# Kernel tuning notes

Hardware: AMD Instinct MI355X
Metric: run time of the kernel (lower is better)

Reference implementation:

```python
import jax, jax.numpy as jnp
import numpy as np

B, S, D, H = 2, 2048, 2048, 32
HD = D // H  # head_dim = 64
NEG = -1e10


def setup_inputs() -> dict:
    key = jax.random.key(0)
    k1, k2, k3 = jax.random.split(key, 3)
    hidden_states = jax.random.normal(k1, (B, S, D), dtype=jnp.float32)
    W = jax.random.normal(k2, (D, 3 * D), dtype=jnp.float32) * (1.0 / np.sqrt(D))
    b = jax.random.normal(k3, (3 * D,), dtype=jnp.float32) * 0.02
    return {"hidden_states": hidden_states, "W": W, "b": b}


def reference(hidden_states, W, b):
    # fused QKV projection: [B,S,D] @ [D,3D] -> [B,S,3D]
    qvk = hidden_states @ W + b
    # OPT interleaved layout: reshape to [B,S,D,3]; channel 0=q, 1=v, 2=k
    qvk = qvk.reshape(B, S, D, 3)
    q = qvk[..., 0].reshape(B, S, H, HD)
    v = qvk[..., 1].reshape(B, S, H, HD)
    k = qvk[..., 2].reshape(B, S, H, HD)
    # causal bias: -1e10 strictly above diagonal, shape [1,1,S,S]
    bias = jnp.triu(jnp.full((S, S), NEG, dtype=jnp.float32), 1)[None, None]
    # dot_product_attention_weights: scale q by 1/sqrt(head_dim)
    scale = jnp.asarray(1.0 / np.sqrt(HD), dtype=jnp.float32)
    scores = jnp.einsum('bqhd,bkhd->bhqk', q * scale, k) + bias  # [B,H,S,S]
    attn_weights = jax.nn.softmax(scores, axis=-1)
    attn_output = jnp.einsum('bhqk,bkhd->bqhd', attn_weights, v)  # [B,S,H,HD]
    return attn_output.reshape(B, S, D)
```

## Files before the change

### kernel.cpp

```cpp
#include <hip/hip_runtime.h>
#include <hip/hip_bf16.h>
#include <stdint.h>

typedef unsigned short ushort_t;
typedef __bf16 bf16x8 __attribute__((ext_vector_type(8)));
typedef float f32x4 __attribute__((ext_vector_type(4)));
typedef float f32x16 __attribute__((ext_vector_type(16)));
typedef int int4v __attribute__((ext_vector_type(4)));
typedef ushort_t ushort8 __attribute__((ext_vector_type(8)));

__device__ __forceinline__ ushort_t f2bf(float f) {
  union { float f; unsigned int u; } v; v.f = f;
  unsigned int r = v.u + 0x7fffu + ((v.u >> 16) & 1u);
  return (ushort_t)(r >> 16);
}

__device__ __forceinline__ bf16x8 ld_bf8(const ushort_t* p) {
  return *reinterpret_cast<const bf16x8*>(p);
}

__device__ __forceinline__ void g2lds16(const void* g, void* l) {
  __builtin_amdgcn_global_load_lds(
      (const __attribute__((address_space(1))) unsigned int*)g,
      (__attribute__((address_space(3))) unsigned int*)l,
      16, 0, 0);
}

__device__ __forceinline__ float ex2(float x) { return __builtin_amdgcn_exp2f(x); }

__device__ __forceinline__ int cvtpk(float a, float b) {
  int r;
  asm("v_cvt_pk_bf16_f32 %0, %1, %2" : "=v"(r) : "v"(a), "v"(b));
  return r;
}

__global__ __launch_bounds__(256) void cvt_hs(const float* __restrict__ in,
                                              ushort_t* __restrict__ out) {
  int i = (blockIdx.x * 256 + threadIdx.x) * 8;
  float4 a = *reinterpret_cast<const float4*>(in + i);
  float4 b = *reinterpret_cast<const float4*>(in + i + 4);
  ushort8 r;
  r[0] = f2bf(a.x); r[1] = f2bf(a.y); r[2] = f2bf(a.z); r[3] = f2bf(a.w);
  r[4] = f2bf(b.x); r[5] = f2bf(b.y); r[6] = f2bf(b.z); r[7] = f2bf(b.w);
  *reinterpret_cast<ushort8*>(out + i) = r;
}

__global__ __launch_bounds__(256) void transpose_W(const float* __restrict__ Win,
                                                   ushort_t* __restrict__ Wt) {
  __shared__ ushort_t T[64][65];
  const int t = threadIdx.x;
  const int k0 = (blockIdx.x & 31) * 64;
  const int n0 = (blockIdx.x >> 5) * 64;
#pragma unroll
  for (int i = 0; i < 16; ++i) {
    int idx = i * 256 + t;
    int r = idx >> 6, c = idx & 63;
    T[r][c] = f2bf(Win[(k0 + r) * 6144 + n0 + c]);
  }
  __syncthreads();
#pragma unroll
  for (int i = 0; i < 16; ++i) {
    int idx = i * 256 + t;
    int nr = idx >> 6, kc = idx & 63;
    Wt[(n0 + nr) * 2048 + k0 + kc] = T[kc][nr];
  }
}

__global__ __launch_bounds__(256, 2) void gemm_qkv(
    const ushort_t* __restrict__ A, const ushort_t* __restrict__ Bt,
    const float* __restrict__ bias,
    ushort_t* __restrict__ Qb, ushort_t* __restrict__ Kb,
    ushort_t* __restrict__ VT) {
  __shared__ __align__(16) char smem[25600];
  ushort_t* As = (ushort_t*)smem;
  ushort_t* Bs = (ushort_t*)(smem + 8192);
  ushort_t* Cs = (ushort_t*)smem;
  const int t = threadIdx.x;
  const int w = t >> 6, l = t & 63;
  const int lo = l & 15, hi = l >> 4;
  const int wr = w >> 1, wc = w & 1;

  int bid = blockIdx.x;
  int swz = (bid & 7) * 128 + (bid >> 3);
  const int mt = swz & 31, nt = swz >> 5;
  const int bm = mt * 128;
  const int bn = nt * 192;

  f32x4 acc[4][6];
#pragma unroll
  for (int i = 0; i < 4; ++i)
#pragma unroll
    for (int j = 0; j < 6; ++j) acc[i][j] = f32x4{0.f, 0.f, 0.f, 0.f};

  const ushort_t* Ag = A + (size_t)bm * 2048;
  const ushort_t* Bg = Bt + (size_t)bn * 2048;

  for (int kk = 0; kk < 2048; kk += 32) {
#pragma unroll
    for (int r2 = 0; r2 < 2; ++r2) {
      int c = r2 * 256 + t;
      int row = c >> 2, s4 = c & 3;
      int slot = s4 ^ ((row & 3) ^ ((row >> 2) & 3));
      g2lds16(Ag + row * 2048 + kk + slot * 8, As + c * 8);
    }
#pragma unroll
    for (int r3 = 0; r3 < 3; ++r3) {
      int c = r3 * 256 + t;
      int row = c >> 2, s4 = c & 3;
      int slot = s4 ^ ((row & 3) ^ ((row >> 2) & 3));
      g2lds16(Bg + row * 2048 + kk + slot * 8, Bs + c * 8);
    }
    __syncthreads();
    bf16x8 af[4], bfr[6];
#pragma unroll
    for (int mf = 0; mf < 4; ++mf) {
      int row = wr * 64 + mf * 16 + lo;
      int fr = (row & 3) ^ ((row >> 2) & 3);
      af[mf] = ld_bf8(As + row * 32 + ((hi ^ fr) << 3));
    }
#pragma unroll
    for (int nf = 0; nf < 6; ++nf) {
      int row = wc * 96 + nf * 16 + lo;
      int fr = (row & 3) ^ ((row >> 2) & 3);
      bfr[nf] = ld_bf8(Bs + row * 32 + ((hi ^ fr) << 3));
    }
    __builtin_amdgcn_s_setprio(1);
#pragma unroll
    for (int mf = 0; mf < 4; ++mf)
#pragma unroll
      for (int nf = 0; nf < 6; ++nf)
        acc[mf][nf] = __builtin_amdgcn_mfma_f32_16x16x32_bf16(
            af[mf], bfr[nf], acc[mf][nf], 0, 0, 0);
    __builtin_amdgcn_s_setprio(0);
    __syncthreads();
  }

  float bv[6];
  int ch[6];
#pragma unroll
  for (int nf = 0; nf < 6; ++nf) {
    int nl = wc * 96 + nf * 16 + lo;
    bv[nf] = bias[bn + nl];
    ch[nf] = nl % 3;
  }
  const int b_ = bm >> 11;
  const int bh = (b_ << 5) + nt;
  const float QS = 0.125f * 1.44269504f;

#pragma unroll
  for (int h = 0; h < 2; ++h) {
    if (wr == h) {
#pragma unroll
      for (int mf = 0; mf < 4; ++mf)
#pragma unroll
        for (int nf = 0; nf < 6; ++nf) {
          int rloc = mf * 16 + hi * 4;
          int nl = wc * 96 + nf * 16 + lo;
          f32x4 a = acc[mf][nf];
#pragma unroll
          for (int j = 0; j < 4; ++j) {
            float v = a[j] + bv[nf];
            if (ch[nf] == 0) v *= QS;
            Cs[(rloc + j) * 200 + nl] = f2bf(v);
          }
        }
    }
    __syncthreads();
    const int sbase = (bm & 2047) + h * 64;
#pragma unroll
    for (int it = 0; it < 2; ++it) {
      int slot = it * 256 + t;
      int r = slot >> 3, g = slot & 7;
      ushort8 vq, vk;
#pragma unroll
      for (int u = 0; u < 8; ++u) {
        int hd = g * 8 + u;
        vq[u] = Cs[r * 200 + hd * 3];
        vk[u] = Cs[r * 200 + hd * 3 + 2];
      }
      size_t rowoff = ((size_t)bh * 2048 + sbase + r) * 64 + g * 8;
      *reinterpret_cast<ushort8*>(Qb + rowoff) = vq;
      *reinterpret_cast<ushort8*>(Kb + rowoff) = vk;
    }
#pragma unroll
    for (int it = 0; it < 2; ++it) {
      int slot = it * 256 + t;
      int hd = slot >> 3, sg = slot & 7;
      ushort8 vv;
#pragma unroll
      for (int u = 0; u < 8; ++u) vv[u] = Cs[(sg * 8 + u) * 200 + hd * 3 + 1];
      *reinterpret_cast<ushort8*>(VT + ((size_t)bh * 64 + hd) * 2048 + sbase +
                                  sg * 8) = vv;
    }
    __syncthreads();
  }
}

__global__ __launch_bounds__(64) void attn(
    const ushort_t* __restrict__ Qb, const ushort_t* __restrict__ Kb,
    const ushort_t* __restrict__ VT, float* __restrict__ out) {
  __shared__ float Ld[32 * 66];
  const int l = threadIdx.x;
  const int ql = l & 31, hi = l >> 5;

  const int bid = blockIdx.x;
  const int bh = bid & 63;
  const int qt = 63 - (bid >> 6);
  const int q0 = qt * 32;
  const int nch = qt + 1;

  const ushort_t* qp = Qb + (bh * 2048 + q0 + ql) * 64 + hi * 8;
  bf16x8 qf[4];
#pragma unroll
  for (int dc = 0; dc < 4; ++dc) qf[dc] = ld_bf8(qp + dc * 16);

  f32x16 o0, o1;
#pragma unroll
  for (int r = 0; r < 16; ++r) { o0[r] = 0.f; o1[r] = 0.f; }
  float mr = -1e30f, lr = 0.f;

  const ushort_t* kbase = Kb + bh * 2048 * 64 + hi * 8;
  const ushort_t* vbase = VT + (bh * 64 + ql) * 2048 + hi * 8;

  bf16x8 kf[4], vf0[2], vf1[2];
  {
    const ushort_t* kp = kbase + ql * 64;
#pragma unroll
    for (int dc = 0; dc < 4; ++dc) kf[dc] = ld_bf8(kp + dc * 16);
#pragma unroll
    for (int s = 0; s < 2; ++s) {
      const ushort_t* vp = vbase + s * 16;
      vf0[s] = ld_bf8(vp);
      vf1[s] = ld_bf8(vp + 32 * 2048);
    }
  }

  for (int c = 0; c < nch; ++c) {
    const int cn = (c + 1 < nch) ? (c + 1) : c;
    const ushort_t* kpn = kbase + (cn * 32 + ql) * 64;
    bf16x8 kn[4], vn0[2], vn1[2];
#pragma unroll
    for (int dc = 0; dc < 4; ++dc) kn[dc] = ld_bf8(kpn + dc * 16);
#pragma unroll
    for (int s = 0; s < 2; ++s) {
      const ushort_t* vpn = vbase + cn * 32 + s * 16;
      vn0[s] = ld_bf8(vpn);
      vn1[s] = ld_bf8(vpn + 32 * 2048);
    }

    f32x16 p;
#pragma unroll
    for (int r = 0; r < 16; ++r) p[r] = 0.f;
    __builtin_amdgcn_s_setprio(1);
#pragma unroll
    for (int dc = 0; dc < 4; ++dc)
      p = __builtin_amdgcn_mfma_f32_32x32x16_bf16(kf[dc], qf[dc], p, 0, 0, 0);
    __builtin_amdgcn_s_setprio(0);
    if (c == nch - 1) {
#pragma unroll
      for (int r = 0; r < 16; ++r) {
        int kvr = (r & 3) + 8 * (r >> 2) + 4 * hi;
        if (kvr > ql) p[r] = -1e30f;
      }
    }
    float mx = p[0];
#pragma unroll
    for (int r = 1; r < 16; ++r) mx = fmaxf(mx, p[r]);
    mx = fmaxf(mx, __shfl_xor(mx, 32));
    if (__any(mx > mr + 10.0f)) {
      float mn = fmaxf(mr, mx);
      float scl = ex2(mr - mn);
      mr = mn;
      lr *= scl;
#pragma unroll
      for (int r = 0; r < 16; ++r) { o0[r] *= scl; o1[r] *= scl; }
    }
    float sum = 0.f;
#pragma unroll
    for (int r = 0; r < 16; ++r) {
      p[r] = ex2(p[r] - mr);
      sum += p[r];
    }
    sum += __shfl_xor(sum, 32);
    lr += sum;

    __builtin_amdgcn_s_setprio(1);
#pragma unroll
    for (int s = 0; s < 2; ++s) {
      int x0 = cvtpk(p[8 * s + 0], p[8 * s + 1]);
      int x1 = cvtpk(p[8 * s + 2], p[8 * s + 3]);
      int y0 = cvtpk(p[8 * s + 4], p[8 * s + 5]);
      int y1 = cvtpk(p[8 * s + 6], p[8 * s + 7]);
      int ox0 = __shfl_xor(x0, 32);
      int ox1 = __shfl_xor(x1, 32);
      int oy0 = __shfl_xor(y0, 32);
      int oy1 = __shfl_xor(y1, 32);
      int4v wv;
      wv[0] = hi ? oy0 : x0;
      wv[1] = hi ? oy1 : x1;
      wv[2] = hi ? y0 : ox0;
      wv[3] = hi ? y1 : ox1;
      bf16x8 pf = __builtin_bit_cast(bf16x8, wv);
      o0 = __builtin_amdgcn_mfma_f32_32x32x16_bf16(vf0[s], pf, o0, 0, 0, 0);
      o1 = __builtin_amdgcn_mfma_f32_32x32x16_bf16(vf1[s], pf, o1, 0, 0, 0);
    }
    __builtin_amdgcn_s_setprio(0);
#pragma unroll
    for (int dc = 0; dc < 4; ++dc) kf[dc] = kn[dc];
#pragma unroll
    for (int s = 0; s < 2; ++s) {
      vf0[s] = vn0[s];
      vf1[s] = vn1[s];
    }
  }

  const float inv = 1.0f / lr;
#pragma unroll
  for (int r = 0; r < 16; ++r) {
    int hdv = (r & 3) + 8 * (r >> 2) + 4 * hi;
    Ld[ql * 66 + hdv] = o0[r] * inv;
    Ld[ql * 66 + 32 + hdv] = o1[r] * inv;
  }
  __syncthreads();
  const int b_ = bh >> 5, h = bh & 31;
  float* op = out + (size_t)(b_ * 2048 + q0) * 2048 + h * 64 + l;
#pragma unroll
  for (int i = 0; i < 32; ++i) {
    op[(size_t)i * 2048] = Ld[i * 66 + l];
  }
}

extern "C" void kernel_launch(void* const* d_in, const int* in_sizes, int n_in,
                              void* d_out, int out_size, void* d_ws,
                              size_t ws_size, hipStream_t stream) {
  (void)in_sizes; (void)n_in; (void)out_size; (void)ws_size;
  const float* hs = (const float*)d_in[0];
  const float* W = (const float*)d_in[1];
  const float* bias = (const float*)d_in[2];
  float* out = (float*)d_out;

  char* ws = (char*)d_ws;
  ushort_t* Abf = (ushort_t*)(ws);
  ushort_t* Wt = (ushort_t*)(ws + (16u << 20));
  ushort_t* Qb = (ushort_t*)(ws + (40u << 20));
  ushort_t* Kb = (ushort_t*)(ws + (56u << 20));
  ushort_t* VT = (ushort_t*)(ws + (72u << 20));

  hipLaunchKernelGGL(cvt_hs, dim3(4096), dim3(256), 0, stream, hs, Abf);
  hipLaunchKernelGGL(transpose_W, dim3(3072), dim3(256), 0, stream, W, Wt);
  hipLaunchKernelGGL(gemm_qkv, dim3(1024), dim3(256), 0, stream, Abf, Wt, bias,
                     Qb, Kb, VT);
  hipLaunchKernelGGL(attn, dim3(4096), dim3(64), 0, stream, Qb, Kb, VT, out);
}
```

Before: 271.3 us.

## Double-buffer QKV GEMM LDS and software-pipeline QK with softmax/PV in attention

```diff
diff --git a/kernel.cpp b/kernel.cpp
--- a/kernel.cpp
+++ b/kernel.cpp
@@ -71,9 +71,11 @@
     const float* __restrict__ bias,
     ushort_t* __restrict__ Qb, ushort_t* __restrict__ Kb,
     ushort_t* __restrict__ VT) {
-  __shared__ __align__(16) char smem[25600];
-  ushort_t* As = (ushort_t*)smem;
-  ushort_t* Bs = (ushort_t*)(smem + 8192);
+  __shared__ __align__(16) char smem[40960];
+  ushort_t* A0 = (ushort_t*)smem;
+  ushort_t* A1 = (ushort_t*)(smem + 8192);
+  ushort_t* B0 = (ushort_t*)(smem + 16384);
+  ushort_t* B1 = (ushort_t*)(smem + 28672);
   ushort_t* Cs = (ushort_t*)smem;
   const int t = threadIdx.x;
   const int w = t >> 6, l = t & 63;
@@ -95,34 +97,40 @@
   const ushort_t* Ag = A + (size_t)bm * 2048;
   const ushort_t* Bg = Bt + (size_t)bn * 2048;
 
+#define STAGE(Ad, Bd, kk_)                                       \
+  do {                                                           \
+    for (int r2 = 0; r2 < 2; ++r2) {                             \
+      int c_ = r2 * 256 + t;                                     \
+      int row_ = c_ >> 2, s4_ = c_ & 3;                          \
+      int slot_ = s4_ ^ ((row_ & 3) ^ ((row_ >> 2) & 3));        \
+      g2lds16(Ag + row_ * 2048 + (kk_) + slot_ * 8, (Ad) + c_ * 8); \
+    }                                                            \
+    for (int r3 = 0; r3 < 3; ++r3) {                             \
+      int c_ = r3 * 256 + t;                                     \
+      int row_ = c_ >> 2, s4_ = c_ & 3;                          \
+      int slot_ = s4_ ^ ((row_ & 3) ^ ((row_ >> 2) & 3));        \
+      g2lds16(Bg + row_ * 2048 + (kk_) + slot_ * 8, (Bd) + c_ * 8); \
+    }                                                            \
+  } while (0)
+
+  STAGE(A0, B0, 0);
+  __syncthreads();
+  ushort_t *Ac = A0, *Bc = B0, *An = A1, *Bn = B1;
+
   for (int kk = 0; kk < 2048; kk += 32) {
-#pragma unroll
-    for (int r2 = 0; r2 < 2; ++r2) {
-      int c = r2 * 256 + t;
-      int row = c >> 2, s4 = c & 3;
-      int slot = s4 ^ ((row & 3) ^ ((row >> 2) & 3));
-      g2lds16(Ag + row * 2048 + kk + slot * 8, As + c * 8);
-    }
-#pragma unroll
-    for (int r3 = 0; r3 < 3; ++r3) {
-      int c = r3 * 256 + t;
-      int row = c >> 2, s4 = c & 3;
-      int slot = s4 ^ ((row & 3) ^ ((row >> 2) & 3));
-      g2lds16(Bg + row * 2048 + kk + slot * 8, Bs + c * 8);
-    }
-    __syncthreads();
+    if (kk + 32 < 2048) STAGE(An, Bn, kk + 32);
     bf16x8 af[4], bfr[6];
 #pragma unroll
     for (int mf = 0; mf < 4; ++mf) {
       int row = wr * 64 + mf * 16 + lo;
       int fr = (row & 3) ^ ((row >> 2) & 3);
-      af[mf] = ld_bf8(As + row * 32 + ((hi ^ fr) << 3));
+      af[mf] = ld_bf8(Ac + row * 32 + ((hi ^ fr) << 3));
     }
 #pragma unroll
     for (int nf = 0; nf < 6; ++nf) {
       int row = wc * 96 + nf * 16 + lo;
       int fr = (row & 3) ^ ((row >> 2) & 3);
-      bfr[nf] = ld_bf8(Bs + row * 32 + ((hi ^ fr) << 3));
+      bfr[nf] = ld_bf8(Bc + row * 32 + ((hi ^ fr) << 3));
     }
     __builtin_amdgcn_s_setprio(1);
 #pragma unroll
@@ -133,7 +141,11 @@
             af[mf], bfr[nf], acc[mf][nf], 0, 0, 0);
     __builtin_amdgcn_s_setprio(0);
     __syncthreads();
-  }
+    ushort_t* tmp;
+    tmp = Ac; Ac = An; An = tmp;
+    tmp = Bc; Bc = Bn; Bn = tmp;
+  }
+#undef STAGE
 
   float bv[6];
   int ch[6];
@@ -196,6 +208,95 @@
   }
 }
 
+__device__ __forceinline__ void ldk(const ushort_t* kbase, int c, int ql,
+                                    bf16x8 k[4]) {
+  const ushort_t* kp = kbase + (c * 32 + ql) * 64;
+#pragma unroll
+  for (int dc = 0; dc < 4; ++dc) k[dc] = ld_bf8(kp + dc * 16);
+}
+
+__device__ __forceinline__ void ldv(const ushort_t* vbase, int c, bf16x8 v0[2],
+                                    bf16x8 v1[2]) {
+  const ushort_t* vp = vbase + c * 32;
+#pragma unroll
+  for (int s = 0; s < 2; ++s) {
+    v0[s] = ld_bf8(vp + s * 16);
+    v1[s] = ld_bf8(vp + s * 16 + 32 * 2048);
+  }
+}
+
+__device__ __forceinline__ f32x16 qk_mfma(const bf16x8 k[4], const bf16x8 q[4]) {
+  f32x16 p;
+#pragma unroll
+  for (int r = 0; r < 16; ++r) p[r] = 0.f;
+  __builtin_amdgcn_s_setprio(1);
+#pragma unroll
+  for (int dc = 0; dc < 4; ++dc)
+    p = __builtin_amdgcn_mfma_f32_32x32x16_bf16(k[dc], q[dc], p, 0, 0, 0);
+  __builtin_amdgcn_s_setprio(0);
+  return p;
+}
+
+__device__ __forceinline__ void sm_pv(f32x16& p, const bf16x8 v0[2],
+                                      const bf16x8 v1[2], f32x16& o0,
+                                      f32x16& o1, float& mr, float& lr,
+                                      bool diag, int ql, int hi) {
+  if (diag) {
+#pragma unroll
+    for (int r = 0; r < 16; ++r) {
+      int kvr = (r & 3) + 8 * (r >> 2) + 4 * hi;
+      if (kvr > ql) p[r] = -1e30f;
+    }
+  }
+  float a0 = fmaxf(p[0], p[1]), a1 = fmaxf(p[2], p[3]);
+  float a2 = fmaxf(p[4], p[5]), a3 = fmaxf(p[6], p[7]);
+  float a4 = fmaxf(p[8], p[9]), a5 = fmaxf(p[10], p[11]);
+  float a6 = fmaxf(p[12], p[13]), a7 = fmaxf(p[14], p[15]);
+  float b0 = fmaxf(a0, a1), b1 = fmaxf(a2, a3);
+  float b2 = fmaxf(a4, a5), b3 = fmaxf(a6, a7);
+  float mx = fmaxf(fmaxf(b0, b1), fmaxf(b2, b3));
+  mx = fmaxf(mx, __shfl_xor(mx, 32));
+  if (__any(mx > mr + 10.0f)) {
+    float mn = fmaxf(mr, mx);
+    float scl = ex2(mr - mn);
+    mr = mn;
+    lr *= scl;
+#pragma unroll
+    for (int r = 0; r < 16; ++r) { o0[r] *= scl; o1[r] *= scl; }
+  }
+#pragma unroll
+  for (int r = 0; r < 16; ++r) p[r] = ex2(p[r] - mr);
+  float s0 = (p[0] + p[1]) + (p[2] + p[3]);
+  float s1 = (p[4] + p[5]) + (p[6] + p[7]);
+  float s2 = (p[8] + p[9]) + (p[10] + p[11]);
+  float s3 = (p[12] + p[13]) + (p[14] + p[15]);
+  float sum = (s0 + s1) + (s2 + s3);
+  sum += __shfl_xor(sum, 32);
+  lr += sum;
+
+  __builtin_amdgcn_s_setprio(1);
+#pragma unroll
+  for (int s = 0; s < 2; ++s) {
+    int x0 = cvtpk(p[8 * s + 0], p[8 * s + 1]);
+    int x1 = cvtpk(p[8 * s + 2], p[8 * s + 3]);
+    int y0 = cvtpk(p[8 * s + 4], p[8 * s + 5]);
+    int y1 = cvtpk(p[8 * s + 6], p[8 * s + 7]);
+    int ox0 = __shfl_xor(x0, 32);
+    int ox1 = __shfl_xor(x1, 32);
+    int oy0 = __shfl_xor(y0, 32);
+    int oy1 = __shfl_xor(y1, 32);
+    int4v wv;
+    wv[0] = hi ? oy0 : x0;
+    wv[1] = hi ? oy1 : x1;
+    wv[2] = hi ? y0 : ox0;
+    wv[3] = hi ? y1 : ox1;
+    bf16x8 pf = __builtin_bit_cast(bf16x8, wv);
+    o0 = __builtin_amdgcn_mfma_f32_32x32x16_bf16(v0[s], pf, o0, 0, 0, 0);
+    o1 = __builtin_amdgcn_mfma_f32_32x32x16_bf16(v1[s], pf, o1, 0, 0, 0);
+  }
+  __builtin_amdgcn_s_setprio(0);
+}
+
 __global__ __launch_bounds__(64) void attn(
     const ushort_t* __restrict__ Qb, const ushort_t* __restrict__ Kb,
     const ushort_t* __restrict__ VT, float* __restrict__ out) {
@@ -222,96 +323,43 @@
   const ushort_t* kbase = Kb + bh * 2048 * 64 + hi * 8;
   const ushort_t* vbase = VT + (bh * 64 + ql) * 2048 + hi * 8;
 
-  bf16x8 kf[4], vf0[2], vf1[2];
+  bf16x8 kA[4], kB[4], vA0[2], vA1[2], vB0[2], vB1[2];
+  f32x16 pA, pB;
+
+  ldk(kbase, 0, ql, kA);
+  ldv(vbase, 0, vA0, vA1);
+  pA = qk_mfma(kA, qf);
   {
-    const ushort_t* kp = kbase + ql * 64;
-#pragma unroll
-    for (int dc = 0; dc < 4; ++dc) kf[dc] = ld_bf8(kp + dc * 16);
-#pragma unroll
-    for (int s = 0; s < 2; ++s) {
-      const ushort_t* vp = vbase + s * 16;
-      vf0[s] = ld_bf8(vp);
-      vf1[s] = ld_bf8(vp + 32 * 2048);
-    }
-  }
-
-  for (int c = 0; c < nch; ++c) {
-    const int cn = (c + 1 < nch) ? (c + 1) : c;
-    const ushort_t* kpn = kbase + (cn * 32 + ql) * 64;
-    bf16x8 kn[4], vn0[2], vn1[2];
-#pragma unroll
-    for (int dc = 0; dc < 4; ++dc) kn[dc] = ld_bf8(kpn + dc * 16);
-#pragma unroll
-    for (int s = 0; s < 2; ++s) {
-      const ushort_t* vpn = vbase + cn * 32 + s * 16;
-      vn0[s] = ld_bf8(vpn);
-      vn1[s] = ld_bf8(vpn + 32 * 2048);
-    }
-
-    f32x16 p;
-#pragma unroll
-    for (int r = 0; r < 16; ++r) p[r] = 0.f;
-    __builtin_amdgcn_s_setprio(1);
-#pragma unroll
-    for (int dc = 0; dc < 4; ++dc)
-      p = __builtin_amdgcn_mfma_f32_32x32x16_bf16(kf[dc], qf[dc], p, 0, 0, 0);
-    __builtin_amdgcn_s_setprio(0);
-    if (c == nch - 1) {
-#pragma unroll
-      for (int r = 0; r < 16; ++r) {
-        int kvr = (r & 3) + 8 * (r >> 2) + 4 * hi;
-        if (kvr > ql) p[r] = -1e30f;
-      }
-    }
-    float mx = p[0];
-#pragma unroll
-    for (int r = 1; r < 16; ++r) mx = fmaxf(mx, p[r]);
-    mx = fmaxf(mx, __shfl_xor(mx, 32));
-    if (__any(mx > mr + 10.0f)) {
-      float mn = fmaxf(mr, mx);
-      float scl = ex2(mr - mn);
-      mr = mn;
-      lr *= scl;
-#pragma unroll
-      for (int r = 0; r < 16; ++r) { o0[r] *= scl; o1[r] *= scl; }
-    }
-    float sum = 0.f;
-#pragma unroll
-    for (int r = 0; r < 16; ++r) {
-      p[r] = ex2(p[r] - mr);
-      sum += p[r];
-    }
-    sum += __shfl_xor(sum, 32);
-    lr += sum;
-
-    __builtin_amdgcn_s_setprio(1);
-#pragma unroll
-    for (int s = 0; s < 2; ++s) {
-      int x0 = cvtpk(p[8 * s + 0], p[8 * s + 1]);
-      int x1 = cvtpk(p[8 * s + 2], p[8 * s + 3]);
-      int y0 = cvtpk(p[8 * s + 4], p[8 * s + 5]);
-      int y1 = cvtpk(p[8 * s + 6], p[8 * s + 7]);
-      int ox0 = __shfl_xor(x0, 32);
-      int ox1 = __shfl_xor(x1, 32);
-      int oy0 = __shfl_xor(y0, 32);
-      int oy1 = __shfl_xor(y1, 32);
-      int4v wv;
-      wv[0] = hi ? oy0 : x0;
-      wv[1] = hi ? oy1 : x1;
-      wv[2] = hi ? y0 : ox0;
-      wv[3] = hi ? y1 : ox1;
-      bf16x8 pf = __builtin_bit_cast(bf16x8, wv);
-      o0 = __builtin_amdgcn_mfma_f32_32x32x16_bf16(vf0[s], pf, o0, 0, 0, 0);
-      o1 = __builtin_amdgcn_mfma_f32_32x32x16_bf16(vf1[s], pf, o1, 0, 0, 0);
-    }
-    __builtin_amdgcn_s_setprio(0);
-#pragma unroll
-    for (int dc = 0; dc < 4; ++dc) kf[dc] = kn[dc];
-#pragma unroll
-    for (int s = 0; s < 2; ++s) {
-      vf0[s] = vn0[s];
-      vf1[s] = vn1[s];
-    }
+    const int c1 = (nch > 1) ? 1 : 0;
+    ldk(kbase, c1, ql, kB);
+    ldv(vbase, c1, vB0, vB1);
+  }
+
+  int c = 0;
+  for (; c + 2 <= nch; c += 2) {
+    pB = qk_mfma(kB, qf);
+    {
+      const int cp = (c + 2 < nch) ? c + 2 : c;
+      ldk(kbase, cp, ql, kA);
+    }
+    sm_pv(pA, vA0, vA1, o0, o1, mr, lr, false, ql, hi);
+    {
+      const int cp = (c + 2 < nch) ? c + 2 : c;
+      ldv(vbase, cp, vA0, vA1);
+    }
+    if (c + 2 < nch) pA = qk_mfma(kA, qf);
+    {
+      const int cp = (c + 3 < nch) ? c + 3 : c;
+      ldk(kbase, cp, ql, kB);
+    }
+    sm_pv(pB, vB0, vB1, o0, o1, mr, lr, (c + 1 == nch - 1), ql, hi);
+    {
+      const int cp = (c + 3 < nch) ? c + 3 : c;
+      ldv(vbase, cp, vB0, vB1);
+    }
+  }
+  if (c < nch) {
+    sm_pv(pA, vA0, vA1, o0, o1, mr, lr, true, ql, hi);
   }
 
   const float inv = 1.0f / lr;
```

Result: no change. 269.7 us (-0.6%).

## Double-buffer QKV GEMM LDS tiles and trim softmax cross-lane reductions

Applied to the files above, without the earlier changes.

```diff
diff --git a/kernel.cpp b/kernel.cpp
--- a/kernel.cpp
+++ b/kernel.cpp
@@ -71,9 +71,11 @@
     const float* __restrict__ bias,
     ushort_t* __restrict__ Qb, ushort_t* __restrict__ Kb,
     ushort_t* __restrict__ VT) {
-  __shared__ __align__(16) char smem[25600];
-  ushort_t* As = (ushort_t*)smem;
-  ushort_t* Bs = (ushort_t*)(smem + 8192);
+  __shared__ __align__(16) char smem[40960];
+  ushort_t* A0 = (ushort_t*)smem;
+  ushort_t* A1 = (ushort_t*)(smem + 8192);
+  ushort_t* B0 = (ushort_t*)(smem + 16384);
+  ushort_t* B1 = (ushort_t*)(smem + 28672);
   ushort_t* Cs = (ushort_t*)smem;
   const int t = threadIdx.x;
   const int w = t >> 6, l = t & 63;
@@ -95,34 +97,40 @@
   const ushort_t* Ag = A + (size_t)bm * 2048;
   const ushort_t* Bg = Bt + (size_t)bn * 2048;
 
+#define STAGE(Ad, Bd, kk_)                                       \
+  do {                                                           \
+    for (int r2 = 0; r2 < 2; ++r2) {                             \
+      int c_ = r2 * 256 + t;                                     \
+      int row_ = c_ >> 2, s4_ = c_ & 3;                          \
+      int slot_ = s4_ ^ ((row_ & 3) ^ ((row_ >> 2) & 3));        \
+      g2lds16(Ag + row_ * 2048 + (kk_) + slot_ * 8, (Ad) + c_ * 8); \
+    }                                                            \
+    for (int r3 = 0; r3 < 3; ++r3) {                             \
+      int c_ = r3 * 256 + t;                                     \
+      int row_ = c_ >> 2, s4_ = c_ & 3;                          \
+      int slot_ = s4_ ^ ((row_ & 3) ^ ((row_ >> 2) & 3));        \
+      g2lds16(Bg + row_ * 2048 + (kk_) + slot_ * 8, (Bd) + c_ * 8); \
+    }                                                            \
+  } while (0)
+
+  STAGE(A0, B0, 0);
+  __syncthreads();
+  ushort_t *Ac = A0, *Bc = B0, *An = A1, *Bn = B1;
+
   for (int kk = 0; kk < 2048; kk += 32) {
-#pragma unroll
-    for (int r2 = 0; r2 < 2; ++r2) {
-      int c = r2 * 256 + t;
-      int row = c >> 2, s4 = c & 3;
-      int slot = s4 ^ ((row & 3) ^ ((row >> 2) & 3));
-      g2lds16(Ag + row * 2048 + kk + slot * 8, As + c * 8);
-    }
-#pragma unroll
-    for (int r3 = 0; r3 < 3; ++r3) {
-      int c = r3 * 256 + t;
-      int row = c >> 2, s4 = c & 3;
-      int slot = s4 ^ ((row & 3) ^ ((row >> 2) & 3));
-      g2lds16(Bg + row * 2048 + kk + slot * 8, Bs + c * 8);
-    }
-    __syncthreads();
+    if (kk + 32 < 2048) STAGE(An, Bn, kk + 32);
     bf16x8 af[4], bfr[6];
 #pragma unroll
     for (int mf = 0; mf < 4; ++mf) {
       int row = wr * 64 + mf * 16 + lo;
       int fr = (row & 3) ^ ((row >> 2) & 3);
-      af[mf] = ld_bf8(As + row * 32 + ((hi ^ fr) << 3));
+      af[mf] = ld_bf8(Ac + row * 32 + ((hi ^ fr) << 3));
     }
 #pragma unroll
     for (int nf = 0; nf < 6; ++nf) {
       int row = wc * 96 + nf * 16 + lo;
       int fr = (row & 3) ^ ((row >> 2) & 3);
-      bfr[nf] = ld_bf8(Bs + row * 32 + ((hi ^ fr) << 3));
+      bfr[nf] = ld_bf8(Bc + row * 32 + ((hi ^ fr) << 3));
     }
     __builtin_amdgcn_s_setprio(1);
 #pragma unroll
@@ -133,7 +141,11 @@
             af[mf], bfr[nf], acc[mf][nf], 0, 0, 0);
     __builtin_amdgcn_s_setprio(0);
     __syncthreads();
-  }
+    ushort_t* tmp;
+    tmp = Ac; Ac = An; An = tmp;
+    tmp = Bc; Bc = Bn; Bn = tmp;
+  }
+#undef STAGE
 
   float bv[6];
   int ch[6];
@@ -263,11 +275,14 @@
         if (kvr > ql) p[r] = -1e30f;
       }
     }
-    float mx = p[0];
-#pragma unroll
-    for (int r = 1; r < 16; ++r) mx = fmaxf(mx, p[r]);
-    mx = fmaxf(mx, __shfl_xor(mx, 32));
+    float a0 = fmaxf(p[0], p[1]), a1 = fmaxf(p[2], p[3]);
+    float a2 = fmaxf(p[4], p[5]), a3 = fmaxf(p[6], p[7]);
+    float a4 = fmaxf(p[8], p[9]), a5 = fmaxf(p[10], p[11]);
+    float a6 = fmaxf(p[12], p[13]), a7 = fmaxf(p[14], p[15]);
+    float mx = fmaxf(fmaxf(fmaxf(a0, a1), fmaxf(a2, a3)),
+                     fmaxf(fmaxf(a4, a5), fmaxf(a6, a7)));
     if (__any(mx > mr + 10.0f)) {
+      mx = fmaxf(mx, __shfl_xor(mx, 32));
       float mn = fmaxf(mr, mx);
       float scl = ex2(mr - mn);
       mr = mn;
@@ -275,14 +290,13 @@
 #pragma unroll
       for (int r = 0; r < 16; ++r) { o0[r] *= scl; o1[r] *= scl; }
     }
-    float sum = 0.f;
-#pragma unroll
-    for (int r = 0; r < 16; ++r) {
-      p[r] = ex2(p[r] - mr);
-      sum += p[r];
-    }
-    sum += __shfl_xor(sum, 32);
-    lr += sum;
+#pragma unroll
+    for (int r = 0; r < 16; ++r) p[r] = ex2(p[r] - mr);
+    float s0 = (p[0] + p[1]) + (p[2] + p[3]);
+    float s1 = (p[4] + p[5]) + (p[6] + p[7]);
+    float s2 = (p[8] + p[9]) + (p[10] + p[11]);
+    float s3 = (p[12] + p[13]) + (p[14] + p[15]);
+    lr += (s0 + s1) + (s2 + s3);
 
     __builtin_amdgcn_s_setprio(1);
 #pragma unroll
@@ -314,7 +328,8 @@
     }
   }
 
-  const float inv = 1.0f / lr;
+  const float lrf = lr + __shfl_xor(lr, 32);
+  const float inv = 1.0f / lrf;
 #pragma unroll
   for (int r = 0; r < 16; ++r) {
     int hdv = (r & 3) + 8 * (r >> 2) + 4 * hi;
```

After: 263.4 us. 2.9% less time.
